# Kernel tuning notes

Measured on AMD Instinct MI355X. Metric: run time of the kernel, lower is better.

Reference implementation:

```python
import jax, jax.numpy as jnp
import numpy as np

B, S, D = 4, 2048, 1024  # batch, seq_len, d_model (h=16 but unused due to source bug)


def setup_inputs() -> dict:
    key = jax.random.key(0)
    ks = jax.random.split(key, 12)
    scale = 1.0 / np.sqrt(D)
    return {
        "q": jax.random.normal(ks[0], (B, S, D), jnp.float32),
        "k": jax.random.normal(ks[1], (B, S, D), jnp.float32),
        "v": jax.random.normal(ks[2], (B, S, D), jnp.float32),
        "mask": jnp.ones((1, 1, S, S), dtype=bool),
        "Wq": jax.random.normal(ks[3], (D, D), jnp.float32) * scale,
        "bq": jnp.zeros((D,), jnp.float32),
        "Wk": jax.random.normal(ks[4], (D, D), jnp.float32) * scale,
        "bk": jnp.zeros((D,), jnp.float32),
        "Wv": jax.random.normal(ks[5], (D, D), jnp.float32) * scale,
        "bv": jnp.zeros((D,), jnp.float32),
        "Wo": jax.random.normal(ks[6], (D, D), jnp.float32) * scale,
        "bo": jnp.zeros((D,), jnp.float32),
    }


def reference(q, k, v, mask, Wq, bq, Wk, bk, Wv, bv, Wo, bo):
    # Faithful to source bugs: head split discarded (attention over full d_model),
    # mask discarded (masked_fill out-of-place), dropout=0 (identity).
    query = q @ Wq + bq  # [B,S,D]
    key = k @ Wk + bk
    value = v @ Wv + bv
    d_k = query.shape[-1]  # = d_model due to the bug
    scores = jnp.einsum('bqd,bkd->bqk', query, key) / jnp.sqrt(jnp.float32(d_k))
    attn = jax.nn.softmax(scores, axis=-1)  # [B,S,S]
    x = jnp.einsum('bqk,bkd->bqd', attn, value)  # [B,S,D]
    # source: x.transpose(1,2).contiguous().view(B,-1,D) -> layout permutation
    b, s, d = x.shape
    x = jnp.swapaxes(x, 1, 2).reshape(b, s, d)
    return x @ Wo + bo
```

## Files before the change

kernel.cpp:

```cpp
#include <hip/hip_runtime.h>
#include <hip/hip_bf16.h>
#include <stdint.h>

typedef __attribute__((ext_vector_type(8))) short short8;
typedef __attribute__((ext_vector_type(4))) float f32x4;
typedef const __attribute__((address_space(1))) uint32_t* gas1_t;
typedef __attribute__((address_space(3))) uint32_t* las3_t;

__device__ __forceinline__ short f2bf(float f) {
  uint32_t u = __builtin_bit_cast(uint32_t, f);
  u += 0x7fffu + ((u >> 16) & 1u);
  return (short)(u >> 16);
}
__device__ __forceinline__ float bf2f(short s) {
  return __builtin_bit_cast(float, ((uint32_t)(uint16_t)s) << 16);
}

__global__ __launch_bounds__(256) void cvt_qkv_k(const float* __restrict__ q,
    const float* __restrict__ k, const float* __restrict__ v,
    short* __restrict__ dst) {
  const long long n = 8388608LL;
  const float* src = (blockIdx.z == 0) ? q : (blockIdx.z == 1) ? k : v;
  long long i = ((long long)blockIdx.x * 256 + threadIdx.x) * 8;
  float4 a = *(const float4*)(src + i);
  float4 b = *(const float4*)(src + i + 4);
  short8 o;
  o[0]=f2bf(a.x); o[1]=f2bf(a.y); o[2]=f2bf(a.z); o[3]=f2bf(a.w);
  o[4]=f2bf(b.x); o[5]=f2bf(b.y); o[6]=f2bf(b.z); o[7]=f2bf(b.w);
  *(short8*)(dst + (long long)blockIdx.z * n + i) = o;
}

__global__ __launch_bounds__(256) void bias_gather_k(const float* b0, const float* b1,
    const float* b2, const float* b3, float* __restrict__ dst) {
  int i = blockIdx.x * 256 + threadIdx.x;
  if (i >= 4096) return;
  int z = i >> 10, j = i & 1023;
  const float* s = (z==0)?b0:(z==1)?b1:(z==2)?b2:b3;
  dst[i] = s[j];
}

__global__ __launch_bounds__(256) void wt_cvt_k(const float* w0, const float* w1,
    const float* w2, const float* w3, short* __restrict__ dst) {
  __shared__ float t[32][33];
  const float* W = (blockIdx.z==0)?w0:(blockIdx.z==1)?w1:(blockIdx.z==2)?w2:w3;
  short* D = dst + (long long)blockIdx.z * 1048576LL;
  int n0 = blockIdx.x * 32, k0 = blockIdx.y * 32;
  int tx = threadIdx.x, ty = threadIdx.y;
  #pragma unroll
  for (int i = 0; i < 4; ++i)
    t[ty + 8*i][tx] = W[(long long)(k0 + ty + 8*i) * 1024 + n0 + tx];
  __syncthreads();
  #pragma unroll
  for (int i = 0; i < 4; ++i)
    D[(long long)(n0 + ty + 8*i) * 1024 + k0 + tx] = f2bf(t[tx][ty + 8*i]);
}

__global__ __launch_bounds__(256) void softmax_bf_k(short* __restrict__ SP) {
  short* sp = SP + (long long)blockIdx.x * 2048;
  const int t = threadIdx.x;
  short8 sv = *(const short8*)(sp + t*8);
  float v[8];
  #pragma unroll
  for (int j = 0; j < 8; ++j) v[j] = bf2f(sv[j]);
  float m = v[0];
  #pragma unroll
  for (int j = 1; j < 8; ++j) m = fmaxf(m, v[j]);
  #pragma unroll
  for (int off = 32; off > 0; off >>= 1) m = fmaxf(m, __shfl_down(m, off, 64));
  __shared__ float rmax[4], rsum[4];
  int wv = t >> 6, ln = t & 63;
  if (ln == 0) rmax[wv] = m;
  __syncthreads();
  m = fmaxf(fmaxf(rmax[0], rmax[1]), fmaxf(rmax[2], rmax[3]));
  float e[8], sum = 0.f;
  #pragma unroll
  for (int j = 0; j < 8; ++j) { e[j] = exp2f((v[j] - m) * 1.44269504f); sum += e[j]; }
  #pragma unroll
  for (int off = 32; off > 0; off >>= 1) sum += __shfl_down(sum, off, 64);
  if (ln == 0) rsum[wv] = sum;
  __syncthreads();
  float inv = 1.0f / (rsum[0] + rsum[1] + rsum[2] + rsum[3]);
  short8 o;
  #pragma unroll
  for (int j = 0; j < 8; ++j) o[j] = f2bf(e[j] * inv);
  *(short8*)(sp + t*8) = o;
}

#define MFMA16(d, a_, b_) d = __builtin_amdgcn_mfma_f32_16x16x32_bf16(a_, b_, d, 0, 0, 0)
#define LGKM0 do { asm volatile("s_waitcnt lgkmcnt(0)" ::: "memory"); \
                   __builtin_amdgcn_sched_barrier(0); } while (0)
#define XCD_DECODE(gxs_, gys_) \
  const int nwg = (int)gridDim.x; \
  const int wg = ((int)blockIdx.x & 7) * (nwg >> 3) + ((int)blockIdx.x >> 3); \
  const int bxi = wg & ((1 << (gxs_)) - 1); \
  const int byi = (wg >> (gxs_)) & ((1 << (gys_)) - 1); \
  const int z = wg >> ((gxs_) + (gys_));

template<int OUT_BF16>
__global__ __launch_bounds__(512, 2) void gemm8_k(const short* __restrict__ A,
    const short* __restrict__ Bt, void* __restrict__ Cv,
    const float* __restrict__ bias,
    int M, int N, int K, long long sA, long long sB, long long sC,
    long long sBias, float scale, int gxs, int gys)
{
  __shared__ __align__(16) short lds[2][2][256*64];
  XCD_DECODE(gxs, gys);
  A  += (long long)z * sA;
  Bt += (long long)z * sB;
  const int bm = byi * 256;
  const int bn = bxi * 256;
  const int tid  = threadIdx.x;
  const int w    = tid >> 6, lane = tid & 63;
  const int wr   = w >> 2,   wc   = w & 3;
  const int lr   = lane & 15, lk  = lane >> 4;

  const int rsw0 = ((lk    ) ^ (lr & 7)) * 8;
  const int rsw1 = ((lk + 4) ^ (lr & 7)) * 8;
  const int srow = w * 8 + (lane >> 3);
  const int swc  = ((lane & 7) ^ ((lane >> 3) & 7)) * 8;
  const short* gA[4]; const short* gB[4];
  #pragma unroll
  for (int i = 0; i < 4; ++i) {
    gA[i] = A  + (long long)(bm + i*64 + srow) * K + swc;
    gB[i] = Bt + (long long)(bn + i*64 + srow) * K + swc;
  }

  #define STG(buf, ab, i, kt) \
    __builtin_amdgcn_global_load_lds((gas1_t)(((ab) ? gB : gA)[i] + (long long)(kt)*64), \
        (las3_t)&lds[buf][ab][(i)*4096 + w*512], 16, 0, 0)
  #define RDA(buf, mi, ks) (*(const short8*)&lds[buf][0][(wr*128 + (mi)*16 + lr)*64 + ((ks) ? rsw1 : rsw0)])
  #define RDB(buf, ni, ks) (*(const short8*)&lds[buf][1][(wc*64  + (ni)*16 + lr)*64 + ((ks) ? rsw1 : rsw0)])

  f32x4 acc[8][4] = {};
  const int nt = K >> 6;

  #pragma unroll
  for (int i = 0; i < 4; ++i) STG(0, 0, i, 0);
  #pragma unroll
  for (int i = 0; i < 4; ++i) STG(0, 1, i, 0);
  STG(1, 0, 0, 1); STG(1, 0, 2, 1);
  STG(1, 1, 0, 1); STG(1, 1, 1, 1);
  STG(1, 1, 2, 1); STG(1, 1, 3, 1);
  asm volatile("s_waitcnt vmcnt(6)" ::: "memory");
  __builtin_amdgcn_s_barrier();

  for (int g = 0; g < nt; ++g) {
    const int b = g & 1, nb = b ^ 1;
    short8 aR[4][2], bR[4][2];
    #pragma unroll
    for (int mi = 0; mi < 4; ++mi) { aR[mi][0] = RDA(b, mi, 0); aR[mi][1] = RDA(b, mi, 1); }
    #pragma unroll
    for (int ni = 0; ni < 2; ++ni) { bR[ni][0] = RDB(b, ni, 0); bR[ni][1] = RDB(b, ni, 1); }
    if (g + 1 < nt) { STG(nb, 0, 1, g+1); STG(nb, 0, 3, g+1); }
    __builtin_amdgcn_s_barrier();
    LGKM0;
    __builtin_amdgcn_s_setprio(1);
    #pragma unroll
    for (int mi = 0; mi < 4; ++mi)
      #pragma unroll
      for (int ni = 0; ni < 2; ++ni) {
        MFMA16(acc[mi][ni], aR[mi][0], bR[ni][0]);
        MFMA16(acc[mi][ni], aR[mi][1], bR[ni][1]);
      }
    __builtin_amdgcn_s_setprio(0);
    __builtin_amdgcn_s_barrier();
    #pragma unroll
    for (int ni = 2; ni < 4; ++ni) { bR[ni][0] = RDB(b, ni, 0); bR[ni][1] = RDB(b, ni, 1); }
    if (g + 2 < nt) { STG(b, 0, 0, g+2); STG(b, 0, 2, g+2); }
    __builtin_amdgcn_s_barrier();
    LGKM0;
    __builtin_amdgcn_s_setprio(1);
    #pragma unroll
    for (int mi = 0; mi < 4; ++mi)
      #pragma unroll
      for (int ni = 2; ni < 4; ++ni) {
        MFMA16(acc[mi][ni], aR[mi][0], bR[ni][0]);
        MFMA16(acc[mi][ni], aR[mi][1], bR[ni][1]);
      }
    __builtin_amdgcn_s_setprio(0);
    __builtin_amdgcn_s_barrier();
    #pragma unroll
    for (int mi = 0; mi < 4; ++mi) { aR[mi][0] = RDA(b, mi+4, 0); aR[mi][1] = RDA(b, mi+4, 1); }
    if (g + 2 < nt) { STG(b, 1, 0, g+2); STG(b, 1, 1, g+2); }
    __builtin_amdgcn_s_barrier();
    LGKM0;
    __builtin_amdgcn_s_setprio(1);
    #pragma unroll
    for (int mi = 0; mi < 4; ++mi)
      #pragma unroll
      for (int ni = 0; ni < 2; ++ni) {
        MFMA16(acc[mi+4][ni], aR[mi][0], bR[ni][0]);
        MFMA16(acc[mi+4][ni], aR[mi][1], bR[ni][1]);
      }
    __builtin_amdgcn_s_setprio(0);
    __builtin_amdgcn_s_barrier();
    if (g + 2 < nt) { STG(b, 1, 2, g+2); STG(b, 1, 3, g+2); }
    __builtin_amdgcn_s_setprio(1);
    #pragma unroll
    for (int mi = 0; mi < 4; ++mi)
      #pragma unroll
      for (int ni = 2; ni < 4; ++ni) {
        MFMA16(acc[mi+4][ni], aR[mi][0], bR[ni][0]);
        MFMA16(acc[mi+4][ni], aR[mi][1], bR[ni][1]);
      }
    __builtin_amdgcn_s_setprio(0);
    if (g + 1 < nt) {
      if (g + 2 < nt) asm volatile("s_waitcnt vmcnt(6)" ::: "memory");
      else            asm volatile("s_waitcnt vmcnt(0)" ::: "memory");
    }
    __builtin_amdgcn_s_barrier();
  }

  const float* bz = bias ? (bias + (long long)z * sBias) : nullptr;
  #pragma unroll
  for (int mi = 0; mi < 8; ++mi) {
    const int row = bm + wr*128 + mi*16 + lk*4;
    #pragma unroll
    for (int ni = 0; ni < 4; ++ni) {
      const int col = bn + wc*64 + ni*16 + lr;
      const float bval = bz ? bz[col] : 0.f;
      #pragma unroll
      for (int r = 0; r < 4; ++r) {
        float val = acc[mi][ni][r] * scale + bval;
        if (OUT_BF16)
          ((short*)Cv)[(long long)z*sC + (long long)(row + r) * N + col] = f2bf(val);
        else
          ((float*)Cv)[(long long)z*sC + (long long)(row + r) * N + col] = val;
      }
    }
  }
  #undef STG
  #undef RDA
  #undef RDB
}

template<int OUT_BF16, int BIAS_ROW>
__global__ __launch_bounds__(512, 2) void gemm4_k(const short* __restrict__ A,
    const short* __restrict__ Bt, void* __restrict__ Cv,
    const float* __restrict__ bias,
    int K, int lda, int ldb, int ldc,
    long long sA, long long sB, long long sC, long long sBias,
    float scale, int gxs, int gys)
{
  __shared__ __align__(16) short lds[3][24576];
  XCD_DECODE(gxs, gys);
  A  += (long long)z * sA;
  Bt += (long long)z * sB;
  const int bm = byi * 256;
  const int bn = bxi * 128;
  const int tid  = threadIdx.x;
  const int w    = tid >> 6, lane = tid & 63;
  const int wr   = w >> 1,   wc   = w & 1;
  const int lr   = lane & 15, lk  = lane >> 4;

  const int rsw0 = ((lk    ) ^ (lr & 7)) * 8;
  const int rsw1 = ((lk + 4) ^ (lr & 7)) * 8;
  const int srow = w * 8 + (lane >> 3);
  const int swc  = ((lane & 7) ^ ((lane >> 3) & 7)) * 8;
  const short* gA[4]; const short* gB[2];
  #pragma unroll
  for (int i = 0; i < 4; ++i)
    gA[i] = A + (long long)(bm + i*64 + srow) * lda + swc;
  #pragma unroll
  for (int i = 0; i < 2; ++i)
    gB[i] = Bt + (long long)(bn + i*64 + srow) * ldb + swc;

  #define STGA(buf, i, kt) \
    __builtin_amdgcn_global_load_lds((gas1_t)(gA[i] + (long long)(kt)*64), \
        (las3_t)&lds[buf][(i)*4096 + w*512], 16, 0, 0)
  #define STGB(buf, i, kt) \
    __builtin_amdgcn_global_load_lds((gas1_t)(gB[i] + (long long)(kt)*64), \
        (las3_t)&lds[buf][16384 + (i)*4096 + w*512], 16, 0, 0)
  #define RDA4(buf, mi, ks) (*(const short8*)&lds[buf][(wr*64 + (mi)*16 + lr)*64 + ((ks) ? rsw1 : rsw0)])
  #define RDB4(buf, ni, ks) (*(const short8*)&lds[buf][16384 + (wc*64 + (ni)*16 + lr)*64 + ((ks) ? rsw1 : rsw0)])

  f32x4 acc[4][4] = {};
  const int nt = K >> 6;

  STGA(0, 0, 0); STGA(0, 2, 0); STGB(0, 0, 0);
  STGB(0, 1, 0); STGA(0, 1, 0); STGA(0, 3, 0);
  STGA(1, 0, 1); STGA(1, 2, 1); STGB(1, 0, 1);
  STGB(1, 1, 1); STGA(1, 1, 1); STGA(1, 3, 1);
  asm volatile("s_waitcnt vmcnt(6)" ::: "memory");
  __builtin_amdgcn_s_barrier();

  int b = 0, nb = 2;
  for (int g = 0; g < nt; ++g) {
    short8 aR[4], bR[4];
    #pragma unroll
    for (int mi = 0; mi < 4; ++mi) aR[mi] = RDA4(b, mi, 0);
    #pragma unroll
    for (int ni = 0; ni < 4; ++ni) bR[ni] = RDB4(b, ni, 0);
    if (g + 2 < nt) { STGA(nb, 0, g+2); STGA(nb, 2, g+2); STGB(nb, 0, g+2); }
    LGKM0;
    __builtin_amdgcn_s_setprio(1);
    #pragma unroll
    for (int mi = 0; mi < 4; ++mi)
      #pragma unroll
      for (int ni = 0; ni < 4; ++ni)
        MFMA16(acc[mi][ni], aR[mi], bR[ni]);
    __builtin_amdgcn_s_setprio(0);
    #pragma unroll
    for (int mi = 0; mi < 4; ++mi) aR[mi] = RDA4(b, mi, 1);
    #pragma unroll
    for (int ni = 0; ni < 4; ++ni) bR[ni] = RDB4(b, ni, 1);
    if (g + 2 < nt) { STGB(nb, 1, g+2); STGA(nb, 1, g+2); STGA(nb, 3, g+2); }
    LGKM0;
    __builtin_amdgcn_s_setprio(1);
    #pragma unroll
    for (int mi = 0; mi < 4; ++mi)
      #pragma unroll
      for (int ni = 0; ni < 4; ++ni)
        MFMA16(acc[mi][ni], aR[mi], bR[ni]);
    __builtin_amdgcn_s_setprio(0);
    if (g + 2 < nt)      asm volatile("s_waitcnt vmcnt(6)" ::: "memory");
    else if (g + 1 < nt) asm volatile("s_waitcnt vmcnt(0)" ::: "memory");
    __builtin_amdgcn_s_barrier();
    b  = (b  == 2) ? 0 : b  + 1;
    nb = (nb == 2) ? 0 : nb + 1;
  }

  const float* bz = bias;
  #pragma unroll
  for (int mi = 0; mi < 4; ++mi) {
    const int row = bm + wr*64 + mi*16 + lk*4;
    #pragma unroll
    for (int ni = 0; ni < 4; ++ni) {
      const int col = bn + wc*64 + ni*16 + lr;
      const float bcol = (bz && !BIAS_ROW) ? bz[(long long)z*sBias + col] : 0.f;
      #pragma unroll
      for (int r = 0; r < 4; ++r) {
        float bval = BIAS_ROW ? bz[row + r] : bcol;
        float val = acc[mi][ni][r] * scale + bval;
        if (OUT_BF16)
          ((short*)Cv)[(long long)z*sC + (long long)(row + r) * ldc + col] = f2bf(val);
        else
          ((float*)Cv)[(long long)z*sC + (long long)(row + r) * ldc + col] = val;
      }
    }
  }
  #undef STGA
  #undef STGB
  #undef RDA4
  #undef RDB4
}

extern "C" void kernel_launch(void* const* d_in, const int* in_sizes, int n_in,
                              void* d_out, int out_size, void* d_ws, size_t ws_size,
                              hipStream_t stream) {
  const float* q  = (const float*)d_in[0];
  const float* k  = (const float*)d_in[1];
  const float* v  = (const float*)d_in[2];
  const float* Wq = (const float*)d_in[4];
  const float* bq = (const float*)d_in[5];
  const float* Wk = (const float*)d_in[6];
  const float* bk = (const float*)d_in[7];
  const float* Wv = (const float*)d_in[8];
  const float* bv = (const float*)d_in[9];
  const float* Wo = (const float*)d_in[10];
  const float* bo = (const float*)d_in[11];

  char* w = (char*)d_ws;
  short* Wt     = (short*)(w);
  float* biasb  = (float*)(w + 8388608);
  short* QKV    = (short*)(w + 8404992);
  short* qkvbf  = (short*)(w + 58736640);
  short* P      = (short*)(w + 58736640);
  short* Vt     = (short*)(w + 92291072);
  short* xt     = (short*)(w + 109068288);

  short* Qp = QKV;
  short* Kp = QKV + 8388608LL;
  short* vbf = qkvbf + 16777216LL;

  cvt_qkv_k<<<dim3(4096,1,3), 256, 0, stream>>>(q, k, v, qkvbf);
  bias_gather_k<<<dim3(16), 256, 0, stream>>>(bq, bk, bv, bo, biasb);
  wt_cvt_k<<<dim3(32,32,4), dim3(32,8), 0, stream>>>(Wq, Wk, Wv, Wo, Wt);

  gemm8_k<1><<<256, 512, 0, stream>>>(qkvbf, Wt, QKV, biasb,
      8192, 1024, 1024, 8388608LL, 1048576LL, 8388608LL, 1024LL, 1.0f, 2, 5);

  gemm4_k<1,1><<<256, 512, 0, stream>>>(Wt + 2097152LL, vbf, Vt, biasb + 2048,
      1024, 1024, 1024, 8192, 0LL, 0LL, 0LL, 0LL, 1.0f, 6, 2);

  gemm8_k<1><<<256, 512, 0, stream>>>(Qp, Kp, P, nullptr,
      2048, 2048, 1024, 2097152LL, 2097152LL, 4194304LL, 0LL, 0.03125f, 3, 3);

  softmax_bf_k<<<dim3(8192), 256, 0, stream>>>(P);

  gemm4_k<1,0><<<256, 512, 0, stream>>>(Vt, P, xt, nullptr,
      2048, 8192, 2048, 2048, 2048LL, 4194304LL, 2097152LL, 0LL, 1.0f, 4, 2);

  gemm4_k<0,0><<<256, 512, 0, stream>>>(xt, Wt + 3145728LL, (float*)d_out,
      biasb + 3072, 1024, 1024, 1024, 1024, 2097152LL, 0LL, 2097152LL, 0LL, 1.0f, 3, 3);
}
```

Baseline: 210.4 us.

## Fuse fp32-to-bf16 input conversion into the QKV projection GEMM loads

Removes the standalone pass that converts q/k/v from fp32 to bf16. Two new GEMM kernels instead load the fp32 activations straight from global memory into registers, convert them to bf16, and write them to LDS, while the bf16 operand still uses direct global-to-LDS loads. This drops a full read-and-write of 96MB of intermediate data and one launch. In exchange the GEMMs read twice the bytes per element and spend VALU work and registers on conversion inside the main loop, which can slow the inner pipeline.

```diff
diff --git a/kernel.cpp b/kernel.cpp
--- a/kernel.cpp
+++ b/kernel.cpp
@@ -14,20 +14,6 @@
 }
 __device__ __forceinline__ float bf2f(short s) {
   return __builtin_bit_cast(float, ((uint32_t)(uint16_t)s) << 16);
-}
-
-__global__ __launch_bounds__(256) void cvt_qkv_k(const float* __restrict__ q,
-    const float* __restrict__ k, const float* __restrict__ v,
-    short* __restrict__ dst) {
-  const long long n = 8388608LL;
-  const float* src = (blockIdx.z == 0) ? q : (blockIdx.z == 1) ? k : v;
-  long long i = ((long long)blockIdx.x * 256 + threadIdx.x) * 8;
-  float4 a = *(const float4*)(src + i);
-  float4 b = *(const float4*)(src + i + 4);
-  short8 o;
-  o[0]=f2bf(a.x); o[1]=f2bf(a.y); o[2]=f2bf(a.z); o[3]=f2bf(a.w);
-  o[4]=f2bf(b.x); o[5]=f2bf(b.y); o[6]=f2bf(b.z); o[7]=f2bf(b.w);
-  *(short8*)(dst + (long long)blockIdx.z * n + i) = o;
 }
 
 __global__ __launch_bounds__(256) void bias_gather_k(const float* b0, const float* b1,
@@ -345,6 +331,223 @@
   #undef RDB4
 }
 
+__global__ __launch_bounds__(512, 2) void gemm4_af32_k(
+    const float* __restrict__ A0p, const float* __restrict__ A1p,
+    const short* __restrict__ Bt, short* __restrict__ C,
+    const float* __restrict__ bias,
+    int K, int lda, int ldb, int ldc,
+    long long sB, long long sC, long long sBias,
+    float scale, int gxs, int gys)
+{
+  __shared__ __align__(16) short lds[3][24576];
+  XCD_DECODE(gxs, gys);
+  const float* Af = z ? A1p : A0p;
+  const int bm = byi * 256;
+  const int bn = bxi * 128;
+  const int tid  = threadIdx.x;
+  const int w    = tid >> 6, lane = tid & 63;
+  const int wr   = w >> 1,   wc   = w & 1;
+  const int lr   = lane & 15, lk  = lane >> 4;
+
+  const int rsw0 = ((lk    ) ^ (lr & 7)) * 8;
+  const int rsw1 = ((lk + 4) ^ (lr & 7)) * 8;
+  const int srow = w * 8 + (lane >> 3);
+  const int swc  = ((lane & 7) ^ ((lane >> 3) & 7)) * 8;
+  const float* gAf[4]; const short* gB[2];
+  #pragma unroll
+  for (int i = 0; i < 4; ++i)
+    gAf[i] = Af + (long long)(bm + i*64 + srow) * lda + swc;
+  #pragma unroll
+  for (int i = 0; i < 2; ++i)
+    gB[i] = Bt + (long long)z * sB + (long long)(bn + i*64 + srow) * ldb + swc;
+
+  float4 la[4][2];
+  #define LAF(i, kt) do { const float* p_ = gAf[i] + (long long)(kt)*64; \
+      la[i][0] = *(const float4*)p_; la[i][1] = *(const float4*)(p_ + 4); } while (0)
+  #define WRA(buf, i) do { short8 s_; \
+      s_[0]=f2bf(la[i][0].x); s_[1]=f2bf(la[i][0].y); s_[2]=f2bf(la[i][0].z); s_[3]=f2bf(la[i][0].w); \
+      s_[4]=f2bf(la[i][1].x); s_[5]=f2bf(la[i][1].y); s_[6]=f2bf(la[i][1].z); s_[7]=f2bf(la[i][1].w); \
+      *(short8*)&lds[buf][(i)*4096 + w*512 + lane*8] = s_; } while (0)
+  #define STGBf(buf, i, kt) \
+    __builtin_amdgcn_global_load_lds((gas1_t)(gB[i] + (long long)(kt)*64), \
+        (las3_t)&lds[buf][16384 + (i)*4096 + w*512], 16, 0, 0)
+  #define RDAf(buf, mi, ks) (*(const short8*)&lds[buf][(wr*64 + (mi)*16 + lr)*64 + ((ks) ? rsw1 : rsw0)])
+  #define RDBf(buf, ni, ks) (*(const short8*)&lds[buf][16384 + (wc*64 + (ni)*16 + lr)*64 + ((ks) ? rsw1 : rsw0)])
+
+  f32x4 acc[4][4] = {};
+  const int nt = K >> 6;
+
+  LAF(0, 0); LAF(2, 0); STGBf(0, 0, 0);
+  LAF(1, 0); LAF(3, 0); STGBf(0, 1, 0);
+  WRA(0, 0); WRA(0, 2);
+  WRA(0, 1); WRA(0, 3);
+  LAF(0, 1); LAF(2, 1); STGBf(1, 0, 1);
+  WRA(1, 0); WRA(1, 2);
+  LAF(1, 1); LAF(3, 1); STGBf(1, 1, 1);
+  LGKM0;
+  __builtin_amdgcn_s_barrier();
+
+  int b = 0, nb = 2, pb = 1;
+  for (int g = 0; g < nt; ++g) {
+    short8 aR[4], bR[4];
+    #pragma unroll
+    for (int mi = 0; mi < 4; ++mi) aR[mi] = RDAf(b, mi, 0);
+    #pragma unroll
+    for (int ni = 0; ni < 4; ++ni) bR[ni] = RDBf(b, ni, 0);
+    if (g + 2 < nt) { LAF(0, g+2); LAF(2, g+2); STGBf(nb, 0, g+2); }
+    if (g + 1 < nt) { WRA(pb, 1); WRA(pb, 3); }
+    LGKM0;
+    __builtin_amdgcn_s_setprio(1);
+    #pragma unroll
+    for (int mi = 0; mi < 4; ++mi)
+      #pragma unroll
+      for (int ni = 0; ni < 4; ++ni)
+        MFMA16(acc[mi][ni], aR[mi], bR[ni]);
+    __builtin_amdgcn_s_setprio(0);
+    #pragma unroll
+    for (int mi = 0; mi < 4; ++mi) aR[mi] = RDAf(b, mi, 1);
+    #pragma unroll
+    for (int ni = 0; ni < 4; ++ni) bR[ni] = RDBf(b, ni, 1);
+    if (g + 2 < nt) { LAF(1, g+2); LAF(3, g+2); STGBf(nb, 1, g+2);
+                      WRA(nb, 0); WRA(nb, 2); }
+    LGKM0;
+    __builtin_amdgcn_s_setprio(1);
+    #pragma unroll
+    for (int mi = 0; mi < 4; ++mi)
+      #pragma unroll
+      for (int ni = 0; ni < 4; ++ni)
+        MFMA16(acc[mi][ni], aR[mi], bR[ni]);
+    __builtin_amdgcn_s_setprio(0);
+    if (g + 2 >= nt) asm volatile("s_waitcnt vmcnt(0)" ::: "memory");
+    __builtin_amdgcn_s_barrier();
+    b  = (b  == 2) ? 0 : b  + 1;
+    nb = (nb == 2) ? 0 : nb + 1;
+    pb = (pb == 2) ? 0 : pb + 1;
+  }
+
+  const float* bz = bias + (long long)z * sBias;
+  #pragma unroll
+  for (int mi = 0; mi < 4; ++mi) {
+    const int row = bm + wr*64 + mi*16 + lk*4;
+    #pragma unroll
+    for (int ni = 0; ni < 4; ++ni) {
+      const int col = bn + wc*64 + ni*16 + lr;
+      const float bval = bz[col];
+      #pragma unroll
+      for (int r = 0; r < 4; ++r)
+        C[(long long)z*sC + (long long)(row + r) * ldc + col] = f2bf(acc[mi][ni][r] * scale + bval);
+    }
+  }
+  #undef LAF
+  #undef WRA
+  #undef STGBf
+  #undef RDAf
+  #undef RDBf
+}
+
+__global__ __launch_bounds__(512, 2) void gemm4_bf32_k(
+    const short* __restrict__ A, const float* __restrict__ Btf,
+    short* __restrict__ C, const float* __restrict__ bias,
+    int K, int lda, int ldb, int ldc, float scale, int gxs, int gys)
+{
+  __shared__ __align__(16) short lds[3][24576];
+  XCD_DECODE(gxs, gys);
+  (void)z;
+  const int bm = byi * 256;
+  const int bn = bxi * 128;
+  const int tid  = threadIdx.x;
+  const int w    = tid >> 6, lane = tid & 63;
+  const int wr   = w >> 1,   wc   = w & 1;
+  const int lr   = lane & 15, lk  = lane >> 4;
+
+  const int rsw0 = ((lk    ) ^ (lr & 7)) * 8;
+  const int rsw1 = ((lk + 4) ^ (lr & 7)) * 8;
+  const int srow = w * 8 + (lane >> 3);
+  const int swc  = ((lane & 7) ^ ((lane >> 3) & 7)) * 8;
+  const short* gA[4]; const float* gBf[2];
+  #pragma unroll
+  for (int i = 0; i < 4; ++i)
+    gA[i] = A + (long long)(bm + i*64 + srow) * lda + swc;
+  #pragma unroll
+  for (int i = 0; i < 2; ++i)
+    gBf[i] = Btf + (long long)(bn + i*64 + srow) * ldb + swc;
+
+  float4 lb[2][2];
+  #define LBF(i, kt) do { const float* p_ = gBf[i] + (long long)(kt)*64; \
+      lb[i][0] = *(const float4*)p_; lb[i][1] = *(const float4*)(p_ + 4); } while (0)
+  #define WRB(buf, i) do { short8 s_; \
+      s_[0]=f2bf(lb[i][0].x); s_[1]=f2bf(lb[i][0].y); s_[2]=f2bf(lb[i][0].z); s_[3]=f2bf(lb[i][0].w); \
+      s_[4]=f2bf(lb[i][1].x); s_[5]=f2bf(lb[i][1].y); s_[6]=f2bf(lb[i][1].z); s_[7]=f2bf(lb[i][1].w); \
+      *(short8*)&lds[buf][16384 + (i)*4096 + w*512 + lane*8] = s_; } while (0)
+  #define STGAb(buf, i, kt) \
+    __builtin_amdgcn_global_load_lds((gas1_t)(gA[i] + (long long)(kt)*64), \
+        (las3_t)&lds[buf][(i)*4096 + w*512], 16, 0, 0)
+  #define RDAb(buf, mi, ks) (*(const short8*)&lds[buf][(wr*64 + (mi)*16 + lr)*64 + ((ks) ? rsw1 : rsw0)])
+  #define RDBb(buf, ni, ks) (*(const short8*)&lds[buf][16384 + (wc*64 + (ni)*16 + lr)*64 + ((ks) ? rsw1 : rsw0)])
+
+  f32x4 acc[4][4] = {};
+  const int nt = K >> 6;
+
+  STGAb(0, 0, 0); STGAb(0, 2, 0); LBF(0, 0); LBF(1, 0); STGAb(0, 1, 0); STGAb(0, 3, 0);
+  WRB(0, 0); WRB(0, 1);
+  STGAb(1, 0, 1); STGAb(1, 2, 1); LBF(0, 1); LBF(1, 1); STGAb(1, 1, 1); STGAb(1, 3, 1);
+  WRB(1, 0); WRB(1, 1);
+  LGKM0;
+  __builtin_amdgcn_s_barrier();
+
+  int b = 0, nb = 2;
+  for (int g = 0; g < nt; ++g) {
+    short8 aR[4], bR[4];
+    #pragma unroll
+    for (int mi = 0; mi < 4; ++mi) aR[mi] = RDAb(b, mi, 0);
+    #pragma unroll
+    for (int ni = 0; ni < 4; ++ni) bR[ni] = RDBb(b, ni, 0);
+    if (g + 2 < nt) { STGAb(nb, 0, g+2); STGAb(nb, 2, g+2); LBF(0, g+2); LBF(1, g+2); }
+    LGKM0;
+    __builtin_amdgcn_s_setprio(1);
+    #pragma unroll
+    for (int mi = 0; mi < 4; ++mi)
+      #pragma unroll
+      for (int ni = 0; ni < 4; ++ni)
+        MFMA16(acc[mi][ni], aR[mi], bR[ni]);
+    __builtin_amdgcn_s_setprio(0);
+    #pragma unroll
+    for (int mi = 0; mi < 4; ++mi) aR[mi] = RDAb(b, mi, 1);
+    #pragma unroll
+    for (int ni = 0; ni < 4; ++ni) bR[ni] = RDBb(b, ni, 1);
+    if (g + 2 < nt) { STGAb(nb, 1, g+2); STGAb(nb, 3, g+2); WRB(nb, 0); WRB(nb, 1); }
+    LGKM0;
+    __builtin_amdgcn_s_setprio(1);
+    #pragma unroll
+    for (int mi = 0; mi < 4; ++mi)
+      #pragma unroll
+      for (int ni = 0; ni < 4; ++ni)
+        MFMA16(acc[mi][ni], aR[mi], bR[ni]);
+    __builtin_amdgcn_s_setprio(0);
+    if (g + 2 >= nt) asm volatile("s_waitcnt vmcnt(0)" ::: "memory");
+    __builtin_amdgcn_s_barrier();
+    b  = (b  == 2) ? 0 : b  + 1;
+    nb = (nb == 2) ? 0 : nb + 1;
+  }
+
+  #pragma unroll
+  for (int mi = 0; mi < 4; ++mi) {
+    const int row = bm + wr*64 + mi*16 + lk*4;
+    #pragma unroll
+    for (int ni = 0; ni < 4; ++ni) {
+      const int col = bn + wc*64 + ni*16 + lr;
+      #pragma unroll
+      for (int r = 0; r < 4; ++r)
+        C[(long long)(row + r) * ldc + col] = f2bf(acc[mi][ni][r] * scale + bias[row + r]);
+    }
+  }
+  #undef LBF
+  #undef WRB
+  #undef STGAb
+  #undef RDAb
+  #undef RDBb
+}
+
 extern "C" void kernel_launch(void* const* d_in, const int* in_sizes, int n_in,
                               void* d_out, int out_size, void* d_ws, size_t ws_size,
                               hipStream_t stream) {
@@ -364,24 +567,21 @@
   short* Wt     = (short*)(w);
   float* biasb  = (float*)(w + 8388608);
   short* QKV    = (short*)(w + 8404992);
-  short* qkvbf  = (short*)(w + 58736640);
-  short* P      = (short*)(w + 58736640);
-  short* Vt     = (short*)(w + 92291072);
-  short* xt     = (short*)(w + 109068288);
+  short* P      = (short*)(w + 41959424);
+  short* Vt     = (short*)(w + 75513856);
+  short* xt     = (short*)(w + 92291072);
 
   short* Qp = QKV;
   short* Kp = QKV + 8388608LL;
-  short* vbf = qkvbf + 16777216LL;
-
-  cvt_qkv_k<<<dim3(4096,1,3), 256, 0, stream>>>(q, k, v, qkvbf);
+
   bias_gather_k<<<dim3(16), 256, 0, stream>>>(bq, bk, bv, bo, biasb);
   wt_cvt_k<<<dim3(32,32,4), dim3(32,8), 0, stream>>>(Wq, Wk, Wv, Wo, Wt);
 
-  gemm8_k<1><<<256, 512, 0, stream>>>(qkvbf, Wt, QKV, biasb,
-      8192, 1024, 1024, 8388608LL, 1048576LL, 8388608LL, 1024LL, 1.0f, 2, 5);
-
-  gemm4_k<1,1><<<256, 512, 0, stream>>>(Wt + 2097152LL, vbf, Vt, biasb + 2048,
-      1024, 1024, 1024, 8192, 0LL, 0LL, 0LL, 0LL, 1.0f, 6, 2);
+  gemm4_af32_k<<<512, 512, 0, stream>>>(q, k, Wt, QKV, biasb,
+      1024, 1024, 1024, 1024, 1048576LL, 8388608LL, 1024LL, 1.0f, 3, 5);
+
+  gemm4_bf32_k<<<256, 512, 0, stream>>>(Wt + 2097152LL, v, Vt, biasb + 2048,
+      1024, 1024, 1024, 8192, 1.0f, 6, 2);
 
   gemm8_k<1><<<256, 512, 0, stream>>>(Qp, Kp, P, nullptr,
       2048, 2048, 1024, 2097152LL, 2097152LL, 4194304LL, 0LL, 0.03125f, 3, 3);
```

Result: slower. 229.3 us (+9.0%).
